# Optimization experiments

Measured on AMD Instinct MI355X. Metric: run time of the kernel, lower is better.

## Reference

```python
import jax, jax.numpy as jnp
import numpy as np

CTX, H, ENC, BALL = 256, 128, 128, 2
IN_DIM = 2 + BALL + ENC  # prev_disp(2) + ball(2) + encoding(128)
B, T = 8192, 128


def setup_inputs() -> dict:
    key = jax.random.key(0)
    ks = jax.random.split(key, 16)
    s = lambda fan_in: 1.0 / np.sqrt(fan_in)
    inp = {
        "context": jax.random.normal(ks[0], (B, CTX), jnp.float32),
        "target_encoding": jax.random.normal(ks[1], (B, ENC), jnp.float32),
        "ball_land_xy": jax.random.normal(ks[2], (B, BALL), jnp.float32),
        "max_frames": T,
        # context_to_h / context_to_c
        "Wh": jax.random.uniform(ks[3], (H, CTX), jnp.float32, -s(CTX), s(CTX)),
        "bh": jax.random.uniform(ks[4], (H,), jnp.float32, -s(CTX), s(CTX)),
        "Wc": jax.random.uniform(ks[5], (H, CTX), jnp.float32, -s(CTX), s(CTX)),
        "bc": jax.random.uniform(ks[6], (H,), jnp.float32, -s(CTX), s(CTX)),
        # LSTM (PyTorch gate order: i, f, g, o)
        "W_ih": jax.random.uniform(ks[7], (4 * H, IN_DIM), jnp.float32, -s(H), s(H)),
        "W_hh": jax.random.uniform(ks[8], (4 * H, H), jnp.float32, -s(H), s(H)),
        "b_ih": jax.random.uniform(ks[9], (4 * H,), jnp.float32, -s(H), s(H)),
        "b_hh": jax.random.uniform(ks[10], (4 * H,), jnp.float32, -s(H), s(H)),
        # output head
        "Wo": jax.random.uniform(ks[11], (2, H), jnp.float32, -s(H), s(H)),
        "bo": jax.random.uniform(ks[12], (2,), jnp.float32, -s(H), s(H)),
    }
    return inp


def _decode(context, target_encoding, ball_land_xy, Wh, bh, Wc, bc,
            W_ih, W_hh, b_ih, b_hh, Wo, bo, max_frames):
    h0 = context @ Wh.T + bh                      # (B, H)
    c0 = context @ Wc.T + bc                      # (B, H)
    Bn = context.shape[0]
    # split input weights: first 2 cols act on prev_disp, rest on static [ball, enc]
    W_prev = W_ih[:, :2]                          # (4H, 2)
    W_stat = W_ih[:, 2:]                          # (4H, BALL+ENC)
    static_in = jnp.concatenate([ball_land_xy, target_encoding], axis=-1)
    gate_static = static_in @ W_stat.T + b_ih + b_hh  # (B, 4H), constant per step
    Hn = h0.shape[-1]

    def step(carry, _):
        h, c, prev = carry
        gates = prev @ W_prev.T + h @ W_hh.T + gate_static
        i, f, g, o = jnp.split(gates, 4, axis=-1)
        c = jax.nn.sigmoid(f) * c + jax.nn.sigmoid(i) * jnp.tanh(g)
        h = jax.nn.sigmoid(o) * jnp.tanh(c)
        pred = h @ Wo.T + bo                      # (B, 2)
        prev = jax.lax.stop_gradient(pred)        # matches .detach()
        return (h, c, prev), pred

    prev0 = jnp.zeros((Bn, 2), dtype=context.dtype)
    _, preds = jax.lax.scan(step, (h0, c0, prev0), None, length=max_frames)
    return jnp.transpose(preds, (1, 0, 2))        # (B, T, 2)


def reference(context, target_encoding, ball_land_xy, max_frames,
              Wh, bh, Wc, bc, W_ih, W_hh, b_ih, b_hh, Wo, bo):
    return _decode(context, target_encoding, ball_land_xy, Wh, bh, Wc, bc,
                   W_ih, W_hh, b_ih, b_hh, Wo, bo, max_frames)
```

## Files before the change

kernel.cpp:

```cpp
#include <hip/hip_runtime.h>
#include <hip/hip_bf16.h>


#define HDIM 128
#define CTX_DIM 256
#define T_FRAMES 128
#define BB 32
#define STR 136

typedef __bf16 bf16x8 __attribute__((ext_vector_type(8)));
typedef float  f32x4  __attribute__((ext_vector_type(4)));

union frag_u {
  bf16x8 v;
  unsigned short s[8];
  uint4 u4;
};

#if __has_builtin(__builtin_amdgcn_exp2f)
#define EXP2(x) __builtin_amdgcn_exp2f(x)
#else
#define EXP2(x) __expf((x) * 0.6931471805599453f)
#endif
#define RCP(x) __builtin_amdgcn_rcpf(x)

__device__ __forceinline__ unsigned short f2bf(float x) {
  unsigned u = __builtin_bit_cast(unsigned, x);
  u += 0x7FFFu + ((u >> 16) & 1u);
  return (unsigned short)(u >> 16);
}
__device__ __forceinline__ float bf2f(unsigned short h) {
  unsigned u = ((unsigned)h) << 16;
  return __builtin_bit_cast(float, u);
}
template<int CTRL>
__device__ __forceinline__ float dpp_mov(float x) {
  return __builtin_bit_cast(float,
    __builtin_amdgcn_mov_dpp(__builtin_bit_cast(int, x), CTRL, 0xF, 0xF, true));
}
__device__ __forceinline__ float row_reduce16(float v) {
  v += dpp_mov<0xB1>(v);
  v += dpp_mov<0x4E>(v);
  v += dpp_mov<0x124>(v);
  v += dpp_mov<0x128>(v);
  return v;
}

#define MFMA(a, b, c) __builtin_amdgcn_mfma_f32_16x16x32_bf16((a), (b), (c), 0, 0, 0)

__global__ __launch_bounds__(512, 1) void traj_lstm(
    const float* __restrict__ ctx, const float* __restrict__ enc,
    const float* __restrict__ ball,
    const float* __restrict__ Wh, const float* __restrict__ bh,
    const float* __restrict__ Wc, const float* __restrict__ bc,
    const float* __restrict__ W_ih, const float* __restrict__ W_hh,
    const float* __restrict__ b_ih, const float* __restrict__ b_hh,
    const float* __restrict__ Wo, const float* __restrict__ bo,
    float* __restrict__ outp)
{
  __shared__ __align__(16) __bf16 sh_h[2][BB * STR];
  __shared__ __align__(16) unsigned short sh_sA[BB * 264];
  __shared__ __align__(16) unsigned short sh_sB[BB * 264];
  __shared__ float sh_pw0[8][BB * 2];
  __shared__ float sh_p0[BB * 2];

  const int tid  = threadIdx.x;
  const int w    = tid >> 6;
  const int l    = tid & 63;
  const int q    = l >> 4;
  const int c16  = l & 15;
  const int colH = w * 16 + c16;
  const int rbase = blockIdx.x * BB;

  const float Lc = 1.4426950408889634f;
  const float SG[4] = {Lc, Lc, 2.f * Lc, Lc};
  const float bo0 = bo[0], bo1 = bo[1];
  const float wo0 = Wo[colH], wo1 = Wo[HDIM + colH];

  float wp0[4], wp1[4];
  #pragma unroll
  for (int g = 0; g < 4; ++g) {
    wp0[g] = W_ih[(size_t)(g * HDIM + colH) * 132 + 0];
    wp1[g] = W_ih[(size_t)(g * HDIM + colH) * 132 + 1];
  }

  frag_u Wf[4][4];
  #pragma unroll
  for (int kt = 0; kt < 4; ++kt) {
    const float* w0p = Wo + kt * 32 + q * 8;
    const float* w1p = Wo + HDIM + kt * 32 + q * 8;
    float4 a0 = *(const float4*)w0p, a1 = *(const float4*)(w0p + 4);
    float4 b0 = *(const float4*)w1p, b1 = *(const float4*)(w1p + 4);
    float wo0v[8] = {a0.x, a0.y, a0.z, a0.w, a1.x, a1.y, a1.z, a1.w};
    float wo1v[8] = {b0.x, b0.y, b0.z, b0.w, b1.x, b1.y, b1.z, b1.w};
    #pragma unroll
    for (int g = 0; g < 4; ++g) {
      const float* wr = W_hh + (size_t)(g * HDIM + colH) * HDIM + kt * 32 + q * 8;
      float4 f0 = *(const float4*)wr;
      float4 f1 = *(const float4*)(wr + 4);
      float ff[8] = {f0.x, f0.y, f0.z, f0.w, f1.x, f1.y, f1.z, f1.w};
      #pragma unroll
      for (int j = 0; j < 8; ++j)
        Wf[g][kt].s[j] = f2bf(SG[g] * (ff[j] + wp0[g] * wo0v[j] + wp1[g] * wo1v[j]));
    }
  }

  frag_u WoF[4];
  #pragma unroll
  for (int kt = 0; kt < 4; ++kt) {
    #pragma unroll
    for (int j = 0; j < 8; ++j) {
      float x = (c16 < 2) ? Wo[c16 * HDIM + kt * 32 + q * 8 + j] : 0.f;
      WoF[kt].s[j] = f2bf(x);
    }
  }

  for (int e = tid; e < BB * 256; e += 512) {
    int row = e >> 8, col = e & 255;
    float x = ctx[(size_t)(rbase + row) * CTX_DIM + col];
    unsigned short hb = f2bf(x);
    sh_sA[row * 264 + col] = hb;
    sh_sB[row * 264 + col] = f2bf(x - bf2f(hb));
  }
  __syncthreads();

  float cst[8];
  {
    f32x4 aH[2] = {{0.f,0.f,0.f,0.f},{0.f,0.f,0.f,0.f}};
    f32x4 aC[2] = {{0.f,0.f,0.f,0.f},{0.f,0.f,0.f,0.f}};
    #pragma unroll
    for (int kt = 0; kt < 8; ++kt) {
      frag_u Ahi[2], Alo[2];
      #pragma unroll
      for (int rt = 0; rt < 2; ++rt) {
        Ahi[rt].u4 = *(const uint4*)&sh_sA[(rt * 16 + c16) * 264 + kt * 32 + q * 8];
        Alo[rt].u4 = *(const uint4*)&sh_sB[(rt * 16 + c16) * 264 + kt * 32 + q * 8];
      }
      frag_u bhi, blo;
      {
        const float* wr = Wh + (size_t)colH * CTX_DIM + kt * 32 + q * 8;
        float4 f0 = *(const float4*)wr;
        float4 f1 = *(const float4*)(wr + 4);
        float ff[8] = {f0.x, f0.y, f0.z, f0.w, f1.x, f1.y, f1.z, f1.w};
        #pragma unroll
        for (int j = 0; j < 8; ++j) {
          unsigned short hb = f2bf(ff[j]);
          bhi.s[j] = hb;
          blo.s[j] = f2bf(ff[j] - bf2f(hb));
        }
      }
      #pragma unroll
      for (int rt = 0; rt < 2; ++rt) {
        aH[rt] = MFMA(Ahi[rt].v, bhi.v, aH[rt]);
        aH[rt] = MFMA(Alo[rt].v, bhi.v, aH[rt]);
        aH[rt] = MFMA(Ahi[rt].v, blo.v, aH[rt]);
      }
      {
        const float* wr = Wc + (size_t)colH * CTX_DIM + kt * 32 + q * 8;
        float4 f0 = *(const float4*)wr;
        float4 f1 = *(const float4*)(wr + 4);
        float ff[8] = {f0.x, f0.y, f0.z, f0.w, f1.x, f1.y, f1.z, f1.w};
        #pragma unroll
        for (int j = 0; j < 8; ++j) {
          unsigned short hb = f2bf(ff[j]);
          bhi.s[j] = hb;
          blo.s[j] = f2bf(ff[j] - bf2f(hb));
        }
      }
      #pragma unroll
      for (int rt = 0; rt < 2; ++rt) {
        aC[rt] = MFMA(Ahi[rt].v, bhi.v, aC[rt]);
        aC[rt] = MFMA(Alo[rt].v, bhi.v, aC[rt]);
        aC[rt] = MFMA(Ahi[rt].v, blo.v, aC[rt]);
      }
    }
    float bhv = bh[colH], bcv = bc[colH];
    float pp0[8][2];
    #pragma unroll
    for (int rt = 0; rt < 2; ++rt) {
      #pragma unroll
      for (int r = 0; r < 4; ++r) {
        float h0v = aH[rt][r] + bhv;
        cst[rt * 4 + r] = aC[rt][r] + bcv;
        sh_h[0][(rt * 16 + q * 4 + r) * STR + colH] = (__bf16)h0v;
        pp0[rt * 4 + r][0] = h0v * wo0;
        pp0[rt * 4 + r][1] = h0v * wo1;
      }
    }
    #pragma unroll
    for (int m = 0; m < 8; ++m) {
      pp0[m][0] = row_reduce16(pp0[m][0]);
      pp0[m][1] = row_reduce16(pp0[m][1]);
    }
    if (c16 == 0) {
      #pragma unroll
      for (int rt = 0; rt < 2; ++rt)
        #pragma unroll
        for (int r = 0; r < 4; ++r) {
          sh_pw0[w][(rt * 16 + q * 4 + r) * 2 + 0] = pp0[rt * 4 + r][0];
          sh_pw0[w][(rt * 16 + q * 4 + r) * 2 + 1] = pp0[rt * 4 + r][1];
        }
    }
  }
  __syncthreads();

  for (int e = tid; e < BB * 168; e += 512) {
    int row = e / 168, col = e - row * 168;
    float x = (col < 2) ? ball[(size_t)(rbase + row) * 2 + col]
            : (col < 130) ? enc[(size_t)(rbase + row) * 128 + (col - 2)] : 0.f;
    unsigned short hb = f2bf(x);
    sh_sA[row * 168 + col] = hb;
    sh_sB[row * 168 + col] = f2bf(x - bf2f(hb));
  }
  if (tid < BB * 2) {
    float s = (tid & 1) ? bo1 : bo0;
    #pragma unroll
    for (int w2 = 0; w2 < 8; ++w2) s += sh_pw0[w2][tid];
    sh_p0[tid] = s;
  }
  __syncthreads();

  f32x4 gacc[2][4] = {{{0.f,0.f,0.f,0.f},{0.f,0.f,0.f,0.f},{0.f,0.f,0.f,0.f},{0.f,0.f,0.f,0.f}},
                      {{0.f,0.f,0.f,0.f},{0.f,0.f,0.f,0.f},{0.f,0.f,0.f,0.f},{0.f,0.f,0.f,0.f}}};
  #pragma unroll
  for (int kt = 0; kt < 5; ++kt) {
    frag_u Ahi[2], Alo[2];
    #pragma unroll
    for (int rt = 0; rt < 2; ++rt) {
      Ahi[rt].u4 = *(const uint4*)&sh_sA[(rt * 16 + c16) * 168 + kt * 32 + q * 8];
      Alo[rt].u4 = *(const uint4*)&sh_sB[(rt * 16 + c16) * 168 + kt * 32 + q * 8];
    }
    #pragma unroll
    for (int g = 0; g < 4; ++g) {
      frag_u bhi, blo;
      #pragma unroll
      for (int j = 0; j < 8; ++j) {
        int kk = kt * 32 + q * 8 + j;
        float x = (kk < 130) ? SG[g] * W_ih[(size_t)(g * HDIM + colH) * 132 + 2 + kk] : 0.f;
        unsigned short hb = f2bf(x);
        bhi.s[j] = hb;
        blo.s[j] = f2bf(x - bf2f(hb));
      }
      #pragma unroll
      for (int rt = 0; rt < 2; ++rt) {
        gacc[rt][g] = MFMA(Ahi[rt].v, bhi.v, gacc[rt][g]);
        gacc[rt][g] = MFMA(Alo[rt].v, bhi.v, gacc[rt][g]);
        gacc[rt][g] = MFMA(Ahi[rt].v, blo.v, gacc[rt][g]);
      }
    }
  }
  float wps0[4], wps1[4];
  #pragma unroll
  for (int g = 0; g < 4; ++g) {
    int colG = g * HDIM + colH;
    float bb = SG[g] * (b_ih[colG] + b_hh[colG] + bo0 * wp0[g] + bo1 * wp1[g]);
    #pragma unroll
    for (int rt = 0; rt < 2; ++rt)
      #pragma unroll
      for (int r = 0; r < 4; ++r) gacc[rt][g][r] += bb;
    wps0[g] = SG[g] * wp0[g];
    wps1[g] = SG[g] * wp1[g];
  }

  auto body = [&](int t, int rbuf, bool first) {
    const int wbuf = rbuf ^ 1;

    const __bf16* hp0 = &sh_h[rbuf][c16 * STR];
    const __bf16* hp1 = &sh_h[rbuf][(16 + c16) * STR];
    f32x4 acc[2][4];
    f32x4 accP = {0.f, 0.f, 0.f, 0.f};
    {
      frag_u A0, A1;
      A0.u4 = *(const uint4*)(hp0 + q * 8);
      A1.u4 = *(const uint4*)(hp1 + q * 8);
      #pragma unroll
      for (int g = 0; g < 4; ++g) {
        acc[0][g] = MFMA(A0.v, Wf[g][0].v, gacc[0][g]);
        acc[1][g] = MFMA(A1.v, Wf[g][0].v, gacc[1][g]);
      }
      if (!first && w >= 6)
        accP = MFMA((w == 6 ? A0.v : A1.v), WoF[0].v, accP);
    }
    #pragma unroll
    for (int kt = 1; kt < 4; ++kt) {
      frag_u A0, A1;
      A0.u4 = *(const uint4*)(hp0 + kt * 32 + q * 8);
      A1.u4 = *(const uint4*)(hp1 + kt * 32 + q * 8);
      #pragma unroll
      for (int g = 0; g < 4; ++g) {
        acc[0][g] = MFMA(A0.v, Wf[g][kt].v, acc[0][g]);
        acc[1][g] = MFMA(A1.v, Wf[g][kt].v, acc[1][g]);
      }
      if (!first && w >= 6)
        accP = MFMA((w == 6 ? A0.v : A1.v), WoF[kt].v, accP);
    }
    if (first) {
      #pragma unroll
      for (int rt = 0; rt < 2; ++rt)
        #pragma unroll
        for (int r = 0; r < 4; ++r) {
          float2 p0r = *(const float2*)&sh_p0[(rt * 16 + q * 4 + r) * 2];
          #pragma unroll
          for (int g = 0; g < 4; ++g)
            acc[rt][g][r] -= p0r.x * wps0[g] + p0r.y * wps1[g];
        }
    }
    if (!first && w >= 6 && c16 < 2) {
      const int m0 = (w - 6) * 16 + q * 4;
      const float bov = c16 ? bo1 : bo0;
      #pragma unroll
      for (int r = 0; r < 4; ++r)
        outp[(size_t)(rbase + m0 + r) * (T_FRAMES * 2) + (t - 1) * 2 + c16] = accP[r] + bov;
    }

    #pragma unroll
    for (int rt = 0; rt < 2; ++rt) {
      __bf16* hw = &sh_h[wbuf][rt * 16 * STR + colH];
      #pragma unroll
      for (int r = 0; r < 4; ++r) {
        float ei = EXP2(-acc[rt][0][r]);
        float ef = EXP2(-acc[rt][1][r]);
        float eg = EXP2(-acc[rt][2][r]);
        float eo = EXP2(-acc[rt][3][r]);
        float t1 = (1.f + ei) * (1.f + eg);
        float pf = 1.f + ef;
        float num = cst[rt * 4 + r] * t1 + (1.f - eg) * pf;
        float cv = num * RCP(t1 * pf);
        cst[rt * 4 + r] = cv;
        float cc = fmaxf(cv, -15.f);
        float ec = EXP2(cc * (-2.f * 1.4426950408889634f));
        float hv = (1.f - ec) * RCP((1.f + eo) * (1.f + ec));
        hw[(q * 4 + r) * STR] = (__bf16)hv;
      }
    }
    __syncthreads();
  };

  body(0, 0, true);
  for (int tp = 0; tp < 63; ++tp) {
    body(2 * tp + 1, 1, false);
    body(2 * tp + 2, 0, false);
  }
  body(127, 1, false);

  if (w >= 6) {
    const __bf16* hp = &sh_h[0][((w - 6) * 16 + c16) * STR];
    f32x4 accP = {0.f, 0.f, 0.f, 0.f};
    #pragma unroll
    for (int kt = 0; kt < 4; ++kt) {
      frag_u A;
      A.u4 = *(const uint4*)(hp + kt * 32 + q * 8);
      accP = MFMA(A.v, WoF[kt].v, accP);
    }
    if (c16 < 2) {
      const int m0 = (w - 6) * 16 + q * 4;
      const float bov = c16 ? bo1 : bo0;
      #pragma unroll
      for (int r = 0; r < 4; ++r)
        outp[(size_t)(rbase + m0 + r) * (T_FRAMES * 2) + 127 * 2 + c16] = accP[r] + bov;
    }
  }
}

extern "C" void kernel_launch(void* const* d_in, const int* in_sizes, int n_in,
                              void* d_out, int out_size, void* d_ws, size_t ws_size,
                              hipStream_t stream) {
  (void)in_sizes; (void)n_in; (void)d_ws; (void)ws_size; (void)out_size;
  const float* ctx  = (const float*)d_in[0];
  const float* enc  = (const float*)d_in[1];
  const float* ball = (const float*)d_in[2];
  const float* Wh   = (const float*)d_in[4];
  const float* bh   = (const float*)d_in[5];
  const float* Wc   = (const float*)d_in[6];
  const float* bc   = (const float*)d_in[7];
  const float* W_ih = (const float*)d_in[8];
  const float* W_hh = (const float*)d_in[9];
  const float* b_ih = (const float*)d_in[10];
  const float* b_hh = (const float*)d_in[11];
  const float* Wo   = (const float*)d_in[12];
  const float* bo   = (const float*)d_in[13];
  float* outp = (float*)d_out;

  dim3 grid(256), block(512);
  traj_lstm<<<grid, block, 0, stream>>>(ctx, enc, ball, Wh, bh, Wc, bc,
                                        W_ih, W_hh, b_ih, b_hh, Wo, bo, outp);
}
```

Baseline: 312.6 us.

## Halve rows per block, double grid, move static gates and Wo fragments to LDS

Reduces the batch tile per block from 32 to 16 rows and doubles the grid to 512 blocks, so the 256 CUs each get more than one block. Launch bounds now request 4 blocks per CU. To cut register pressure, the precomputed static gate contributions and the Wo fragments move from registers into shared memory and are reloaded every step. The trade-off is that each block does half the MFMA work per step against the same weight fragments, and each step adds LDS reads for the static gates.

Measured after the change: 358.4 us. 1.15x slower.

```diff
diff --git a/kernel.cpp b/kernel.cpp
--- a/kernel.cpp
+++ b/kernel.cpp
@@ -5,7 +5,7 @@
 #define HDIM 128
 #define CTX_DIM 256
 #define T_FRAMES 128
-#define BB 32
+#define BB 16
 #define STR 136
 
 typedef __bf16 bf16x8 __attribute__((ext_vector_type(8)));
@@ -48,7 +48,7 @@
 
 #define MFMA(a, b, c) __builtin_amdgcn_mfma_f32_16x16x32_bf16((a), (b), (c), 0, 0, 0)
 
-__global__ __launch_bounds__(512, 1) void traj_lstm(
+__global__ __launch_bounds__(512, 4) void traj_lstm(
     const float* __restrict__ ctx, const float* __restrict__ enc,
     const float* __restrict__ ball,
     const float* __restrict__ Wh, const float* __restrict__ bh,
@@ -61,6 +61,8 @@
   __shared__ __align__(16) __bf16 sh_h[2][BB * STR];
   __shared__ __align__(16) unsigned short sh_sA[BB * 264];
   __shared__ __align__(16) unsigned short sh_sB[BB * 264];
+  __shared__ __align__(16) float sh_gs[4 * HDIM * 16];
+  __shared__ __align__(16) uint4 sh_wof[4 * 64];
   __shared__ float sh_pw0[8][BB * 2];
   __shared__ float sh_p0[BB * 2];
 
@@ -105,14 +107,15 @@
     }
   }
 
-  frag_u WoF[4];
   #pragma unroll
   for (int kt = 0; kt < 4; ++kt) {
+    frag_u wf;
     #pragma unroll
     for (int j = 0; j < 8; ++j) {
       float x = (c16 < 2) ? Wo[c16 * HDIM + kt * 32 + q * 8 + j] : 0.f;
-      WoF[kt].s[j] = f2bf(x);
-    }
+      wf.s[j] = f2bf(x);
+    }
+    if (w == 0) sh_wof[kt * 64 + l] = wf.u4;
   }
 
   for (int e = tid; e < BB * 256; e += 512) {
@@ -124,18 +127,15 @@
   }
   __syncthreads();
 
-  float cst[8];
+  float cst[4];
   {
-    f32x4 aH[2] = {{0.f,0.f,0.f,0.f},{0.f,0.f,0.f,0.f}};
-    f32x4 aC[2] = {{0.f,0.f,0.f,0.f},{0.f,0.f,0.f,0.f}};
+    f32x4 aH = {0.f,0.f,0.f,0.f};
+    f32x4 aC = {0.f,0.f,0.f,0.f};
     #pragma unroll
     for (int kt = 0; kt < 8; ++kt) {
-      frag_u Ahi[2], Alo[2];
-      #pragma unroll
-      for (int rt = 0; rt < 2; ++rt) {
-        Ahi[rt].u4 = *(const uint4*)&sh_sA[(rt * 16 + c16) * 264 + kt * 32 + q * 8];
-        Alo[rt].u4 = *(const uint4*)&sh_sB[(rt * 16 + c16) * 264 + kt * 32 + q * 8];
-      }
+      frag_u Ahi, Alo;
+      Ahi.u4 = *(const uint4*)&sh_sA[c16 * 264 + kt * 32 + q * 8];
+      Alo.u4 = *(const uint4*)&sh_sB[c16 * 264 + kt * 32 + q * 8];
       frag_u bhi, blo;
       {
         const float* wr = Wh + (size_t)colH * CTX_DIM + kt * 32 + q * 8;
@@ -149,12 +149,9 @@
           blo.s[j] = f2bf(ff[j] - bf2f(hb));
         }
       }
-      #pragma unroll
-      for (int rt = 0; rt < 2; ++rt) {
-        aH[rt] = MFMA(Ahi[rt].v, bhi.v, aH[rt]);
-        aH[rt] = MFMA(Alo[rt].v, bhi.v, aH[rt]);
-        aH[rt] = MFMA(Ahi[rt].v, blo.v, aH[rt]);
-      }
+      aH = MFMA(Ahi.v, bhi.v, aH);
+      aH = MFMA(Alo.v, bhi.v, aH);
+      aH = MFMA(Ahi.v, blo.v, aH);
       {
         const float* wr = Wc + (size_t)colH * CTX_DIM + kt * 32 + q * 8;
         float4 f0 = *(const float4*)wr;
@@ -167,39 +164,31 @@
           blo.s[j] = f2bf(ff[j] - bf2f(hb));
         }
       }
-      #pragma unroll
-      for (int rt = 0; rt < 2; ++rt) {
-        aC[rt] = MFMA(Ahi[rt].v, bhi.v, aC[rt]);
-        aC[rt] = MFMA(Alo[rt].v, bhi.v, aC[rt]);
-        aC[rt] = MFMA(Ahi[rt].v, blo.v, aC[rt]);
-      }
+      aC = MFMA(Ahi.v, bhi.v, aC);
+      aC = MFMA(Alo.v, bhi.v, aC);
+      aC = MFMA(Ahi.v, blo.v, aC);
     }
     float bhv = bh[colH], bcv = bc[colH];
-    float pp0[8][2];
-    #pragma unroll
-    for (int rt = 0; rt < 2; ++rt) {
-      #pragma unroll
-      for (int r = 0; r < 4; ++r) {
-        float h0v = aH[rt][r] + bhv;
-        cst[rt * 4 + r] = aC[rt][r] + bcv;
-        sh_h[0][(rt * 16 + q * 4 + r) * STR + colH] = (__bf16)h0v;
-        pp0[rt * 4 + r][0] = h0v * wo0;
-        pp0[rt * 4 + r][1] = h0v * wo1;
-      }
-    }
-    #pragma unroll
-    for (int m = 0; m < 8; ++m) {
+    float pp0[4][2];
+    #pragma unroll
+    for (int r = 0; r < 4; ++r) {
+      float h0v = aH[r] + bhv;
+      cst[r] = aC[r] + bcv;
+      sh_h[0][(q * 4 + r) * STR + colH] = (__bf16)h0v;
+      pp0[r][0] = h0v * wo0;
+      pp0[r][1] = h0v * wo1;
+    }
+    #pragma unroll
+    for (int m = 0; m < 4; ++m) {
       pp0[m][0] = row_reduce16(pp0[m][0]);
       pp0[m][1] = row_reduce16(pp0[m][1]);
     }
     if (c16 == 0) {
       #pragma unroll
-      for (int rt = 0; rt < 2; ++rt)
-        #pragma unroll
-        for (int r = 0; r < 4; ++r) {
-          sh_pw0[w][(rt * 16 + q * 4 + r) * 2 + 0] = pp0[rt * 4 + r][0];
-          sh_pw0[w][(rt * 16 + q * 4 + r) * 2 + 1] = pp0[rt * 4 + r][1];
-        }
+      for (int r = 0; r < 4; ++r) {
+        sh_pw0[w][(q * 4 + r) * 2 + 0] = pp0[r][0];
+        sh_pw0[w][(q * 4 + r) * 2 + 1] = pp0[r][1];
+      }
     }
   }
   __syncthreads();
@@ -220,118 +209,102 @@
   }
   __syncthreads();
 
-  f32x4 gacc[2][4] = {{{0.f,0.f,0.f,0.f},{0.f,0.f,0.f,0.f},{0.f,0.f,0.f,0.f},{0.f,0.f,0.f,0.f}},
-                      {{0.f,0.f,0.f,0.f},{0.f,0.f,0.f,0.f},{0.f,0.f,0.f,0.f},{0.f,0.f,0.f,0.f}}};
-  #pragma unroll
-  for (int kt = 0; kt < 5; ++kt) {
-    frag_u Ahi[2], Alo[2];
-    #pragma unroll
-    for (int rt = 0; rt < 2; ++rt) {
-      Ahi[rt].u4 = *(const uint4*)&sh_sA[(rt * 16 + c16) * 168 + kt * 32 + q * 8];
-      Alo[rt].u4 = *(const uint4*)&sh_sB[(rt * 16 + c16) * 168 + kt * 32 + q * 8];
+  {
+    f32x4 gacc[4] = {{0.f,0.f,0.f,0.f},{0.f,0.f,0.f,0.f},
+                     {0.f,0.f,0.f,0.f},{0.f,0.f,0.f,0.f}};
+    #pragma unroll
+    for (int kt = 0; kt < 5; ++kt) {
+      frag_u Ahi, Alo;
+      Ahi.u4 = *(const uint4*)&sh_sA[c16 * 168 + kt * 32 + q * 8];
+      Alo.u4 = *(const uint4*)&sh_sB[c16 * 168 + kt * 32 + q * 8];
+      #pragma unroll
+      for (int g = 0; g < 4; ++g) {
+        frag_u bhi, blo;
+        #pragma unroll
+        for (int j = 0; j < 8; ++j) {
+          int kk = kt * 32 + q * 8 + j;
+          float x = (kk < 130) ? SG[g] * W_ih[(size_t)(g * HDIM + colH) * 132 + 2 + kk] : 0.f;
+          unsigned short hb = f2bf(x);
+          bhi.s[j] = hb;
+          blo.s[j] = f2bf(x - bf2f(hb));
+        }
+        gacc[g] = MFMA(Ahi.v, bhi.v, gacc[g]);
+        gacc[g] = MFMA(Alo.v, bhi.v, gacc[g]);
+        gacc[g] = MFMA(Ahi.v, blo.v, gacc[g]);
+      }
     }
     #pragma unroll
     for (int g = 0; g < 4; ++g) {
-      frag_u bhi, blo;
-      #pragma unroll
-      for (int j = 0; j < 8; ++j) {
-        int kk = kt * 32 + q * 8 + j;
-        float x = (kk < 130) ? SG[g] * W_ih[(size_t)(g * HDIM + colH) * 132 + 2 + kk] : 0.f;
-        unsigned short hb = f2bf(x);
-        bhi.s[j] = hb;
-        blo.s[j] = f2bf(x - bf2f(hb));
-      }
-      #pragma unroll
-      for (int rt = 0; rt < 2; ++rt) {
-        gacc[rt][g] = MFMA(Ahi[rt].v, bhi.v, gacc[rt][g]);
-        gacc[rt][g] = MFMA(Alo[rt].v, bhi.v, gacc[rt][g]);
-        gacc[rt][g] = MFMA(Ahi[rt].v, blo.v, gacc[rt][g]);
-      }
+      int colG = g * HDIM + colH;
+      float bb = SG[g] * (b_ih[colG] + b_hh[colG] + bo0 * wp0[g] + bo1 * wp1[g]);
+      f32x4 t = gacc[g];
+      t[0] += bb; t[1] += bb; t[2] += bb; t[3] += bb;
+      *(f32x4*)&sh_gs[((g * HDIM + colH) * 4 + q) * 4] = t;
     }
   }
   float wps0[4], wps1[4];
   #pragma unroll
   for (int g = 0; g < 4; ++g) {
-    int colG = g * HDIM + colH;
-    float bb = SG[g] * (b_ih[colG] + b_hh[colG] + bo0 * wp0[g] + bo1 * wp1[g]);
-    #pragma unroll
-    for (int rt = 0; rt < 2; ++rt)
-      #pragma unroll
-      for (int r = 0; r < 4; ++r) gacc[rt][g][r] += bb;
     wps0[g] = SG[g] * wp0[g];
     wps1[g] = SG[g] * wp1[g];
   }
 
   auto body = [&](int t, int rbuf, bool first) {
     const int wbuf = rbuf ^ 1;
-
-    const __bf16* hp0 = &sh_h[rbuf][c16 * STR];
-    const __bf16* hp1 = &sh_h[rbuf][(16 + c16) * STR];
-    f32x4 acc[2][4];
+    const __bf16* hp = &sh_h[rbuf][c16 * STR];
+
+    f32x4 acc[4];
+    #pragma unroll
+    for (int g = 0; g < 4; ++g)
+      acc[g] = *(const f32x4*)&sh_gs[((g * HDIM + colH) * 4 + q) * 4];
     f32x4 accP = {0.f, 0.f, 0.f, 0.f};
-    {
-      frag_u A0, A1;
-      A0.u4 = *(const uint4*)(hp0 + q * 8);
-      A1.u4 = *(const uint4*)(hp1 + q * 8);
-      #pragma unroll
-      for (int g = 0; g < 4; ++g) {
-        acc[0][g] = MFMA(A0.v, Wf[g][0].v, gacc[0][g]);
-        acc[1][g] = MFMA(A1.v, Wf[g][0].v, gacc[1][g]);
-      }
-      if (!first && w >= 6)
-        accP = MFMA((w == 6 ? A0.v : A1.v), WoF[0].v, accP);
-    }
-    #pragma unroll
-    for (int kt = 1; kt < 4; ++kt) {
-      frag_u A0, A1;
-      A0.u4 = *(const uint4*)(hp0 + kt * 32 + q * 8);
-      A1.u4 = *(const uint4*)(hp1 + kt * 32 + q * 8);
-      #pragma unroll
-      for (int g = 0; g < 4; ++g) {
-        acc[0][g] = MFMA(A0.v, Wf[g][kt].v, acc[0][g]);
-        acc[1][g] = MFMA(A1.v, Wf[g][kt].v, acc[1][g]);
-      }
-      if (!first && w >= 6)
-        accP = MFMA((w == 6 ? A0.v : A1.v), WoF[kt].v, accP);
+
+    #pragma unroll
+    for (int kt = 0; kt < 4; ++kt) {
+      frag_u A;
+      A.u4 = *(const uint4*)(hp + kt * 32 + q * 8);
+      #pragma unroll
+      for (int g = 0; g < 4; ++g)
+        acc[g] = MFMA(A.v, Wf[g][kt].v, acc[g]);
+      if (!first && w == 7) {
+        frag_u wof;
+        wof.u4 = sh_wof[kt * 64 + l];
+        accP = MFMA(A.v, wof.v, accP);
+      }
     }
     if (first) {
       #pragma unroll
-      for (int rt = 0; rt < 2; ++rt)
+      for (int r = 0; r < 4; ++r) {
+        float2 p0r = *(const float2*)&sh_p0[(q * 4 + r) * 2];
         #pragma unroll
-        for (int r = 0; r < 4; ++r) {
-          float2 p0r = *(const float2*)&sh_p0[(rt * 16 + q * 4 + r) * 2];
-          #pragma unroll
-          for (int g = 0; g < 4; ++g)
-            acc[rt][g][r] -= p0r.x * wps0[g] + p0r.y * wps1[g];
-        }
-    }
-    if (!first && w >= 6 && c16 < 2) {
-      const int m0 = (w - 6) * 16 + q * 4;
+        for (int g = 0; g < 4; ++g)
+          acc[g][r] -= p0r.x * wps0[g] + p0r.y * wps1[g];
+      }
+    }
+    if (!first && w == 7 && c16 < 2) {
+      const int m0 = q * 4;
       const float bov = c16 ? bo1 : bo0;
       #pragma unroll
       for (int r = 0; r < 4; ++r)
         outp[(size_t)(rbase + m0 + r) * (T_FRAMES * 2) + (t - 1) * 2 + c16] = accP[r] + bov;
     }
 
-    #pragma unroll
-    for (int rt = 0; rt < 2; ++rt) {
-      __bf16* hw = &sh_h[wbuf][rt * 16 * STR + colH];
-      #pragma unroll
-      for (int r = 0; r < 4; ++r) {
-        float ei = EXP2(-acc[rt][0][r]);
-        float ef = EXP2(-acc[rt][1][r]);
-        float eg = EXP2(-acc[rt][2][r]);
-        float eo = EXP2(-acc[rt][3][r]);
-        float t1 = (1.f + ei) * (1.f + eg);
-        float pf = 1.f + ef;
-        float num = cst[rt * 4 + r] * t1 + (1.f - eg) * pf;
-        float cv = num * RCP(t1 * pf);
-        cst[rt * 4 + r] = cv;
-        float cc = fmaxf(cv, -15.f);
-        float ec = EXP2(cc * (-2.f * 1.4426950408889634f));
-        float hv = (1.f - ec) * RCP((1.f + eo) * (1.f + ec));
-        hw[(q * 4 + r) * STR] = (__bf16)hv;
-      }
+    __bf16* hw = &sh_h[wbuf][colH];
+    #pragma unroll
+    for (int r = 0; r < 4; ++r) {
+      float ei = EXP2(-acc[0][r]);
+      float ef = EXP2(-acc[1][r]);
+      float eg = EXP2(-acc[2][r]);
+      float eo = EXP2(-acc[3][r]);
+      float t1 = (1.f + ei) * (1.f + eg);
+      float pf = 1.f + ef;
+      float num = cst[r] * t1 + (1.f - eg) * pf;
+      float cv = num * RCP(t1 * pf);
+      cst[r] = cv;
+      float cc = fmaxf(cv, -15.f);
+      float ec = EXP2(cc * (-2.f * 1.4426950408889634f));
+      float hv = (1.f - ec) * RCP((1.f + eo) * (1.f + ec));
+      hw[(q * 4 + r) * STR] = (__bf16)hv;
     }
     __syncthreads();
   };
@@ -343,17 +316,18 @@
   }
   body(127, 1, false);
 
-  if (w >= 6) {
-    const __bf16* hp = &sh_h[0][((w - 6) * 16 + c16) * STR];
+  if (w == 7) {
+    const __bf16* hp = &sh_h[0][c16 * STR];
     f32x4 accP = {0.f, 0.f, 0.f, 0.f};
     #pragma unroll
     for (int kt = 0; kt < 4; ++kt) {
-      frag_u A;
+      frag_u A, wof;
       A.u4 = *(const uint4*)(hp + kt * 32 + q * 8);
-      accP = MFMA(A.v, WoF[kt].v, accP);
+      wof.u4 = sh_wof[kt * 64 + l];
+      accP = MFMA(A.v, wof.v, accP);
     }
     if (c16 < 2) {
-      const int m0 = (w - 6) * 16 + q * 4;
+      const int m0 = q * 4;
       const float bov = c16 ? bo1 : bo0;
       #pragma unroll
       for (int r = 0; r < 4; ++r)
@@ -381,7 +355,7 @@
   const float* bo   = (const float*)d_in[13];
   float* outp = (float*)d_out;
 
-  dim3 grid(256), block(512);
+  dim3 grid(512), block(512);
   traj_lstm<<<grid, block, 0, stream>>>(ctx, enc, ball, Wh, bh, Wc, bc,
                                         W_ih, W_hh, b_ih, b_hh, Wo, bo, outp);
 }
```

## Software-pipeline LSTM step across two row tiles to overlap MFMA with gate math

Applied to the files above, without the earlier changes.

Each timestep is split into two half-phases, one per 16-row tile. The MFMA gate matmul for one tile runs alongside the transcendental elementwise update of the other tile, so the matrix and vector units can work concurrently. This doubles the number of barriers per step, and the final tile's elementwise update is peeled out after the loop. The Wo fragments move from registers into shared memory to lower register pressure, at the cost of extra LDS reads in the prediction path.

Result: no change. 307.1 us (-1.7%).

```diff
diff --git a/kernel.cpp b/kernel.cpp
--- a/kernel.cpp
+++ b/kernel.cpp
@@ -45,6 +45,8 @@
   v += dpp_mov<0x128>(v);
   return v;
 }
+
+template<int N> struct Int { static constexpr int value = N; };
 
 #define MFMA(a, b, c) __builtin_amdgcn_mfma_f32_16x16x32_bf16((a), (b), (c), 0, 0, 0)
 
@@ -61,6 +63,7 @@
   __shared__ __align__(16) __bf16 sh_h[2][BB * STR];
   __shared__ __align__(16) unsigned short sh_sA[BB * 264];
   __shared__ __align__(16) unsigned short sh_sB[BB * 264];
+  __shared__ __align__(16) uint4 sh_wof[4 * 64];
   __shared__ float sh_pw0[8][BB * 2];
   __shared__ float sh_p0[BB * 2];
 
@@ -105,14 +108,15 @@
     }
   }
 
-  frag_u WoF[4];
   #pragma unroll
   for (int kt = 0; kt < 4; ++kt) {
+    frag_u wf;
     #pragma unroll
     for (int j = 0; j < 8; ++j) {
       float x = (c16 < 2) ? Wo[c16 * HDIM + kt * 32 + q * 8 + j] : 0.f;
-      WoF[kt].s[j] = f2bf(x);
-    }
+      wf.s[j] = f2bf(x);
+    }
+    if (w == 0) sh_wof[kt * 64 + l] = wf.u4;
   }
 
   for (int e = tid; e < BB * 256; e += 512) {
@@ -124,7 +128,7 @@
   }
   __syncthreads();
 
-  float cst[8];
+  float cst[2][4];
   {
     f32x4 aH[2] = {{0.f,0.f,0.f,0.f},{0.f,0.f,0.f,0.f}};
     f32x4 aC[2] = {{0.f,0.f,0.f,0.f},{0.f,0.f,0.f,0.f}};
@@ -181,7 +185,7 @@
       #pragma unroll
       for (int r = 0; r < 4; ++r) {
         float h0v = aH[rt][r] + bhv;
-        cst[rt * 4 + r] = aC[rt][r] + bcv;
+        cst[rt][r] = aC[rt][r] + bcv;
         sh_h[0][(rt * 16 + q * 4 + r) * STR + colH] = (__bf16)h0v;
         pp0[rt * 4 + r][0] = h0v * wo0;
         pp0[rt * 4 + r][1] = h0v * wo1;
@@ -262,98 +266,116 @@
     wps1[g] = SG[g] * wp1[g];
   }
 
-  auto body = [&](int t, int rbuf, bool first) {
-    const int wbuf = rbuf ^ 1;
-
-    const __bf16* hp0 = &sh_h[rbuf][c16 * STR];
-    const __bf16* hp1 = &sh_h[rbuf][(16 + c16) * STR];
-    f32x4 acc[2][4];
-    f32x4 accP = {0.f, 0.f, 0.f, 0.f};
-    {
-      frag_u A0, A1;
-      A0.u4 = *(const uint4*)(hp0 + q * 8);
-      A1.u4 = *(const uint4*)(hp1 + q * 8);
-      #pragma unroll
-      for (int g = 0; g < 4; ++g) {
-        acc[0][g] = MFMA(A0.v, Wf[g][0].v, gacc[0][g]);
-        acc[1][g] = MFMA(A1.v, Wf[g][0].v, gacc[1][g]);
-      }
-      if (!first && w >= 6)
-        accP = MFMA((w == 6 ? A0.v : A1.v), WoF[0].v, accP);
-    }
-    #pragma unroll
-    for (int kt = 1; kt < 4; ++kt) {
-      frag_u A0, A1;
-      A0.u4 = *(const uint4*)(hp0 + kt * 32 + q * 8);
-      A1.u4 = *(const uint4*)(hp1 + kt * 32 + q * 8);
-      #pragma unroll
-      for (int g = 0; g < 4; ++g) {
-        acc[0][g] = MFMA(A0.v, Wf[g][kt].v, acc[0][g]);
-        acc[1][g] = MFMA(A1.v, Wf[g][kt].v, acc[1][g]);
-      }
-      if (!first && w >= 6)
-        accP = MFMA((w == 6 ? A0.v : A1.v), WoF[kt].v, accP);
-    }
-    if (first) {
-      #pragma unroll
-      for (int rt = 0; rt < 2; ++rt)
+  f32x4 acc[2][4];
+
+  auto phase = [&](auto GC, int t, bool doEw, bool corr, bool doPred) {
+    constexpr int G = decltype(GC)::value;
+    constexpr int E = 1 - G;
+    const int rbuf = t & 1;
+    const __bf16* hp = &sh_h[rbuf][(G * 16 + c16) * STR];
+
+    frag_u A[4];
+    #pragma unroll
+    for (int kt = 0; kt < 4; ++kt)
+      A[kt].u4 = *(const uint4*)(hp + kt * 32 + q * 8);
+    #pragma unroll
+    for (int g = 0; g < 4; ++g) acc[G][g] = gacc[G][g];
+    #pragma unroll
+    for (int kt = 0; kt < 4; ++kt)
+      #pragma unroll
+      for (int g = 0; g < 4; ++g)
+        acc[G][g] = MFMA(A[kt].v, Wf[g][kt].v, acc[G][g]);
+
+    if (doPred && w == 6 + G) {
+      f32x4 accP = {0.f, 0.f, 0.f, 0.f};
+      #pragma unroll
+      for (int kt = 0; kt < 4; ++kt) {
+        frag_u wof;
+        wof.u4 = sh_wof[kt * 64 + l];
+        accP = MFMA(A[kt].v, wof.v, accP);
+      }
+      if (c16 < 2) {
+        const int m0 = G * 16 + q * 4;
+        const float bov = c16 ? bo1 : bo0;
+        #pragma unroll
+        for (int r = 0; r < 4; ++r)
+          outp[(size_t)(rbase + m0 + r) * (T_FRAMES * 2) + (t - 1) * 2 + c16] = accP[r] + bov;
+      }
+    }
+
+    if (doEw) {
+      if (corr) {
         #pragma unroll
         for (int r = 0; r < 4; ++r) {
-          float2 p0r = *(const float2*)&sh_p0[(rt * 16 + q * 4 + r) * 2];
+          float2 p0r = *(const float2*)&sh_p0[(E * 16 + q * 4 + r) * 2];
           #pragma unroll
           for (int g = 0; g < 4; ++g)
-            acc[rt][g][r] -= p0r.x * wps0[g] + p0r.y * wps1[g];
+            acc[E][g][r] -= p0r.x * wps0[g] + p0r.y * wps1[g];
         }
-    }
-    if (!first && w >= 6 && c16 < 2) {
-      const int m0 = (w - 6) * 16 + q * 4;
-      const float bov = c16 ? bo1 : bo0;
-      #pragma unroll
-      for (int r = 0; r < 4; ++r)
-        outp[(size_t)(rbase + m0 + r) * (T_FRAMES * 2) + (t - 1) * 2 + c16] = accP[r] + bov;
-    }
-
-    #pragma unroll
-    for (int rt = 0; rt < 2; ++rt) {
-      __bf16* hw = &sh_h[wbuf][rt * 16 * STR + colH];
+      }
+      __bf16* hwp = &sh_h[(t + G) & 1][(E * 16) * STR + colH];
       #pragma unroll
       for (int r = 0; r < 4; ++r) {
-        float ei = EXP2(-acc[rt][0][r]);
-        float ef = EXP2(-acc[rt][1][r]);
-        float eg = EXP2(-acc[rt][2][r]);
-        float eo = EXP2(-acc[rt][3][r]);
+        float ei = EXP2(-acc[E][0][r]);
+        float ef = EXP2(-acc[E][1][r]);
+        float eg = EXP2(-acc[E][2][r]);
+        float eo = EXP2(-acc[E][3][r]);
         float t1 = (1.f + ei) * (1.f + eg);
         float pf = 1.f + ef;
-        float num = cst[rt * 4 + r] * t1 + (1.f - eg) * pf;
+        float num = cst[E][r] * t1 + (1.f - eg) * pf;
         float cv = num * RCP(t1 * pf);
-        cst[rt * 4 + r] = cv;
+        cst[E][r] = cv;
         float cc = fmaxf(cv, -15.f);
         float ec = EXP2(cc * (-2.f * 1.4426950408889634f));
         float hv = (1.f - ec) * RCP((1.f + eo) * (1.f + ec));
-        hw[(q * 4 + r) * STR] = (__bf16)hv;
+        hwp[(q * 4 + r) * STR] = (__bf16)hv;
       }
     }
     __syncthreads();
   };
 
-  body(0, 0, true);
-  for (int tp = 0; tp < 63; ++tp) {
-    body(2 * tp + 1, 1, false);
-    body(2 * tp + 2, 0, false);
-  }
-  body(127, 1, false);
-
-  if (w >= 6) {
-    const __bf16* hp = &sh_h[0][((w - 6) * 16 + c16) * STR];
+  phase(Int<0>{}, 0, false, false, false);
+  phase(Int<1>{}, 0, true,  true,  false);
+  phase(Int<0>{}, 1, true,  true,  true);
+  for (int t = 1; t < 127; ++t) {
+    phase(Int<1>{}, t,     true, false, true);
+    phase(Int<0>{}, t + 1, true, false, true);
+  }
+  phase(Int<1>{}, 127, true, false, true);
+
+  {
+    __bf16* hwp = &sh_h[0][16 * STR + colH];
+    #pragma unroll
+    for (int r = 0; r < 4; ++r) {
+      float ei = EXP2(-acc[1][0][r]);
+      float ef = EXP2(-acc[1][1][r]);
+      float eg = EXP2(-acc[1][2][r]);
+      float eo = EXP2(-acc[1][3][r]);
+      float t1 = (1.f + ei) * (1.f + eg);
+      float pf = 1.f + ef;
+      float num = cst[1][r] * t1 + (1.f - eg) * pf;
+      float cv = num * RCP(t1 * pf);
+      float cc = fmaxf(cv, -15.f);
+      float ec = EXP2(cc * (-2.f * 1.4426950408889634f));
+      float hv = (1.f - ec) * RCP((1.f + eo) * (1.f + ec));
+      hwp[(q * 4 + r) * STR] = (__bf16)hv;
+    }
+  }
+  __syncthreads();
+
+  if (w == 6 || w == 7) {
+    const int Ge = w - 6;
+    const __bf16* hp = &sh_h[0][(Ge * 16 + c16) * STR];
     f32x4 accP = {0.f, 0.f, 0.f, 0.f};
     #pragma unroll
     for (int kt = 0; kt < 4; ++kt) {
-      frag_u A;
+      frag_u A, wof;
       A.u4 = *(const uint4*)(hp + kt * 32 + q * 8);
-      accP = MFMA(A.v, WoF[kt].v, accP);
+      wof.u4 = sh_wof[kt * 64 + l];
+      accP = MFMA(A.v, wof.v, accP);
     }
     if (c16 < 2) {
-      const int m0 = (w - 6) * 16 + q * 4;
+      const int m0 = Ge * 16 + q * 4;
       const float bov = c16 ? bo1 : bo0;
       #pragma unroll
       for (int r = 0; r < 4; ++r)
```
